# Kernel optimization log

Measured on AMD Instinct MI355X. Metric: run time of the kernel, lower is better.

Reference implementation:

```python
import jax, jax.numpy as jnp
import numpy as np

N, H = 8192, 128  # nodes, hidden_dim


def setup_inputs() -> dict:
    key = jax.random.key(0)
    ks = jax.random.split(key, 5)
    X = jax.random.normal(ks[0], (N, H), dtype=jnp.float32)
    adj = jax.random.uniform(ks[1], (N, N), dtype=jnp.float32)
    W1 = jax.random.normal(ks[2], (H, H), dtype=jnp.float32) / np.sqrt(H).astype(np.float32)
    b1 = jnp.zeros((H,), jnp.float32)
    W2 = jax.random.normal(ks[3], (H, H), dtype=jnp.float32) / np.sqrt(H).astype(np.float32)
    b2 = jnp.zeros((H,), jnp.float32)
    a = jax.random.normal(ks[4], (2 * H, 1), dtype=jnp.float32) * 0.1
    return {"X": X, "adj": adj, "W1": W1, "b1": b1, "W2": W2, "b2": b2, "a": a}


def reference(X, adj, W1, b1, W2, b2, a):
    n = X.shape[0]
    leaky = jax.nn.leaky_relu  # negative_slope = 0.01, matches torch defaults

    # --- GCN diffusion: A_hat = A + I, symmetric normalization, 3 hops ---
    A_hat = adj + jnp.eye(n, dtype=adj.dtype)
    dinv_sqrt = jax.lax.rsqrt(A_hat.sum(axis=1))
    A_norm = dinv_sqrt[:, None] * A_hat * dinv_sqrt[None, :]
    hA = A_norm @ X
    hA2 = A_norm @ hA
    hA3 = A_norm @ hA2
    hA, hA2, hA3 = leaky(hA), leaky(hA2), leaky(hA3)

    # --- scattering diffusion: lazy walk P = 0.5*(I + A D^-1), wavelets ---
    deg = adj.sum(axis=1)
    AD = adj / deg[None, :]  # A @ D^{-1} (column-normalized)

    def P(v):
        return 0.5 * (v + AD @ v)

    px = P(X)
    p2x = P(px)
    p3x = P(p2x)
    p4x = P(p3x)
    # moment = 1 -> |.|**1
    s1 = jnp.abs(X - px)      # Psi_1 = I - P
    s2 = jnp.abs(px - p2x)    # Psi_2 = P - P^2
    s3 = jnp.abs(p2x - p4x)   # Psi_3 = P^2 - P^4

    # --- 6-way attention fusion ---
    h_all = jnp.stack([hA, hA2, hA3, s1, s2, s3], axis=1)         # [N,6,H]
    h_rep = jnp.broadcast_to(X[:, None, :], h_all.shape)          # [N,6,H]
    a_input = jnp.concatenate([h_rep, h_all], axis=-1)            # [N,6,2H]
    e = jnp.einsum('nsk,ko->ns', jax.nn.relu(a_input), a)         # [N,6]
    attn = jax.nn.softmax(e, axis=1)                              # [N,6]
    h_prime = jnp.mean(attn[:, :, None] * h_all, axis=1)          # [N,H]

    # --- output MLP (Withgres=False, so gres layer is skipped) ---
    out = leaky(h_prime @ W1.T + b1)
    out = leaky(out @ W2.T + b2)
    return out
```

## Files before the change

kernel.cpp:

```cpp
#include <hip/hip_runtime.h>

typedef unsigned short ushort_t;
typedef unsigned int   uint_t;
typedef int   i32x4 __attribute__((ext_vector_type(4)));

typedef __attribute__((address_space(3))) void lds_void_t;
typedef __attribute__((address_space(1))) void gbl_void_t;

#define NN 8192
#define HH 128
#define KS 8
#define KLEN 1024
#define NTQ 16

__device__ __forceinline__ ushort_t f2bf(float x) {
    uint_t u = __float_as_uint(x);
    u += 0x7fffu + ((u >> 16) & 1u);
    return (ushort_t)(u >> 16);
}
__device__ __forceinline__ float bf2f(uint_t lo16) { return __uint_as_float(lo16 << 16); }
__device__ __forceinline__ float leaky(float x) { return x > 0.f ? x : 0.01f * x; }

__global__ __launch_bounds__(256) void conv_rowsum(const float* __restrict__ adj,
    char* __restrict__ adjq, float* __restrict__ s, float* __restrict__ rinv,
    float* __restrict__ zbase)
{
    const int i = blockIdx.x;
    if (i == 0) {
        ((float4*)zbase)[threadIdx.x] = float4{0.f, 0.f, 0.f, 0.f};
    }
    const float4* arow = (const float4*)(adj + ((size_t)i << 13));
    uint_t* brow = (uint_t*)(adjq + ((size_t)i << 13));
    float partial = 0.f;
    for (int t = threadIdx.x; t < 2048; t += 256) {
        const float4 v = arow[t];
        partial += (v.x + v.y) + (v.z + v.w);
        const uint_t q0 = (uint_t)__float2int_rn(v.x * 127.f);
        const uint_t q1 = (uint_t)__float2int_rn(v.y * 127.f);
        const uint_t q2 = (uint_t)__float2int_rn(v.z * 127.f);
        const uint_t q3 = (uint_t)__float2int_rn(v.w * 127.f);
        brow[t] = q0 | (q1 << 8) | (q2 << 16) | (q3 << 24);
    }
    #pragma unroll
    for (int off = 32; off; off >>= 1) partial += __shfl_xor(partial, off);
    __shared__ float ps[4];
    if ((threadIdx.x & 63) == 0) ps[threadIdx.x >> 6] = partial;
    __syncthreads();
    if (threadIdx.x == 0) {
        const float tot = (ps[0] + ps[1]) + (ps[2] + ps[3]);
        s[i]    = rsqrtf(tot + 1.0f);
        rinv[i] = 1.0f / tot;
    }
}

__global__ __launch_bounds__(256) void preMax(const float* __restrict__ u,
    const float* __restrict__ v, const float* __restrict__ s, const float* __restrict__ rinv,
    float* __restrict__ cmax)
{
    const int j0 = (blockIdx.x & 127) << 6;
    const int c0 = (blockIdx.x >> 7) << 6;
    __shared__ uint_t cm[64];
    if (threadIdx.x < 64) cm[threadIdx.x] = 0;
    __syncthreads();
    const int tx = threadIdx.x & 63;
    const int ty = threadIdx.x >> 6;
    float m = 0.f;
    #pragma unroll
    for (int rr = 0; rr < 16; ++rr) {
        const int j = j0 + ty + (rr << 2);
        const int c = c0 + tx;
        const float val = (c < 128) ? s[j] * u[((size_t)j << 7) + c]
                                    : rinv[j] * v[((size_t)j << 7) + (c - 128)];
        m = fmaxf(m, fabsf(val));
    }
    atomicMax(&cm[tx], __float_as_uint(m));
    __syncthreads();
    if (threadIdx.x < 64)
        atomicMax((uint_t*)&cmax[c0 + threadIdx.x], cm[threadIdx.x]);
}

__global__ __launch_bounds__(256) void preQ(const float* __restrict__ u,
    const float* __restrict__ v, const float* __restrict__ s, const float* __restrict__ rinv,
    const float* __restrict__ cmax, char* __restrict__ Bi8, float* __restrict__ dq)
{
    const int j0 = (blockIdx.x & 127) << 6;
    const int c0 = (blockIdx.x >> 7) << 6;
    __shared__ float tile[64][65];
    const int tx = threadIdx.x & 63;
    const int ty = threadIdx.x >> 6;
    #pragma unroll
    for (int rr = 0; rr < 16; ++rr) {
        const int jl = ty + (rr << 2);
        const int j = j0 + jl;
        const int c = c0 + tx;
        tile[jl][tx] = (c < 128) ? s[j] * u[((size_t)j << 7) + c]
                                 : rinv[j] * v[((size_t)j << 7) + (c - 128)];
    }
    __syncthreads();
    const int cl = threadIdx.x & 63;
    const int jq = threadIdx.x >> 6;
    const float cmv = cmax[c0 + cl];
    const float rs = cmv > 0.f ? 127.f / cmv : 0.f;
    uint_t w4[4];
    #pragma unroll
    for (int g = 0; g < 4; ++g) {
        uint_t wv = 0;
        #pragma unroll
        for (int b = 0; b < 4; ++b) {
            int q = __float2int_rn(tile[(jq << 4) + (g << 2) + b][cl] * rs);
            q = q > 127 ? 127 : (q < -127 ? -127 : q);
            wv |= ((uint_t)(q & 0xff)) << (8 * b);
        }
        w4[g] = wv;
    }
    uint4 st; st.x = w4[0]; st.y = w4[1]; st.z = w4[2]; st.w = w4[3];
    *(uint4*)(Bi8 + ((size_t)(c0 + cl) << 13) + j0 + (jq << 4)) = st;
    if ((blockIdx.x & 127) == 0 && threadIdx.x < 64)
        dq[c0 + threadIdx.x] = cmax[c0 + threadIdx.x] * (1.f / 16129.f);
}

#define WAITB(S) do {                                         \
    asm volatile("s_waitcnt " S ::: "memory");                \
    __builtin_amdgcn_sched_barrier(0);                        \
    __builtin_amdgcn_s_barrier();                             \
    __builtin_amdgcn_sched_barrier(0);                        \
} while (0)

__global__ __launch_bounds__(512, 2) void gemm_i8(const char* __restrict__ A,
    const char* __restrict__ Bt, ushort_t* __restrict__ Yb)
{
    __shared__ char lds[4 * 32768];
    const int bid = blockIdx.x;
    const int mb = bid & 31;
    const int ks = bid >> 5;
    const size_t mBase = (size_t)mb * 256;
    const int tid = threadIdx.x;
    const int w = tid >> 6, l = tid & 63;
    const int wr = w >> 2, wc = w & 3;
    const int frow = l & 15, fk = l >> 4;
    const int fsl = ((fk ^ ((frow >> 1) & 3)) << 4);
    const int srow = l >> 2;
    const int skoff = (((l & 3) ^ ((l >> 3) & 3)) << 4);
    const int kBeg = ks << 10;

    i32x4 acc[8][4] = {};

    auto STAGE = [&](int t) {
        const int k0 = kBeg + (t << 6);
        char* base = &lds[(t & 3) << 15];
        #pragma unroll
        for (int q = 0; q < 2; ++q) {
            const int c = (w << 1) + q;
            const int row = (c << 4) + srow;
            __builtin_amdgcn_global_load_lds(
                (const gbl_void_t*)(A + ((mBase + row) << 13) + k0 + skoff),
                (lds_void_t*)(base + (c << 10)), 16, 0, 0);
            __builtin_amdgcn_global_load_lds(
                (const gbl_void_t*)(Bt + ((size_t)row << 13) + k0 + skoff),
                (lds_void_t*)(base + 16384 + (c << 10)), 16, 0, 0);
        }
    };
    auto COMPUTE = [&](int T) {
        const char* buf = &lds[(T & 3) << 15];
        i32x4 av[8], bv[4];
        #pragma unroll
        for (int mi = 0; mi < 8; ++mi) {
            const int row = (wr << 7) + (mi << 4) + frow;
            av[mi] = *(const i32x4*)(buf + (row << 6) + fsl);
        }
        #pragma unroll
        for (int ni = 0; ni < 4; ++ni) {
            const int col = (wc << 6) + (ni << 4) + frow;
            bv[ni] = *(const i32x4*)(buf + 16384 + (col << 6) + fsl);
        }
        __builtin_amdgcn_s_setprio(1);
        #pragma unroll
        for (int mi = 0; mi < 8; ++mi)
            #pragma unroll
            for (int ni = 0; ni < 4; ++ni)
                acc[mi][ni] = __builtin_amdgcn_mfma_i32_16x16x64_i8(
                    av[mi], bv[ni], acc[mi][ni], 0, 0, 0);
        __builtin_amdgcn_s_setprio(0);
    };

    STAGE(0); STAGE(1); STAGE(2);
    #pragma unroll 1
    for (int T = 0; T < NTQ - 3; ++T) {
        WAITB("vmcnt(8)");
        STAGE(T + 3);
        COMPUTE(T);
    }
    WAITB("vmcnt(8)"); COMPUTE(NTQ - 3);
    WAITB("vmcnt(4)"); COMPUTE(NTQ - 2);
    WAITB("vmcnt(0)"); COMPUTE(NTQ - 1);
    __syncthreads();

    ushort_t* Cs = (ushort_t*)lds;
    const int orow = (l >> 4) << 2;
    const int ocol = l & 15;
    #pragma unroll
    for (int mi = 0; mi < 8; ++mi) {
        #pragma unroll
        for (int ni = 0; ni < 4; ++ni) {
            const int rl = (wr << 7) + (mi << 4) + orow;
            const int cl = (wc << 6) + (ni << 4) + ocol;
            #pragma unroll
            for (int r = 0; r < 4; ++r)
                Cs[(rl + r) * 256 + cl] = f2bf((float)acc[mi][ni][r]);
        }
    }
    __syncthreads();
    const size_t sliceBase = ((size_t)ks * NN + mBase) * 256;
    #pragma unroll
    for (int p = 0; p < 16; ++p) {
        const int idx16 = (p << 9) + tid;
        const int row   = idx16 >> 5;
        const int c16   = idx16 & 31;
        const uint4 v = *(const uint4*)(&Cs[(row << 8) + (c16 << 3)]);
        *(uint4*)(Yb + sliceBase + (size_t)row * 256 + (c16 << 3)) = v;
    }
}

__global__ __launch_bounds__(256, 2) void gemm_half_i8(const char* __restrict__ A,
    const char* __restrict__ Bt, ushort_t* __restrict__ Yb, int nbOff, int nbCount)
{
    __shared__ char lds[2 * 24576];
    const int bid  = blockIdx.x;
    const int mb   = bid & 31;
    const int rest = bid >> 5;
    const int nb   = nbOff + (rest % nbCount);
    const int ks   = rest / nbCount;
    const size_t mBase = (size_t)mb * 256;
    const size_t nBase = (size_t)nb * 128;
    const int tid = threadIdx.x;
    const int w = tid >> 6, l = tid & 63;
    const int wr = w >> 1, wc = w & 1;
    const int frow = l & 15, fk = l >> 4;
    const int fsl = ((fk ^ ((frow >> 1) & 3)) << 4);
    const int srow = l >> 2;
    const int skoff = (((l & 3) ^ ((l >> 3) & 3)) << 4);
    const int kBeg = ks << 10;

    i32x4 acc[8][4] = {};

    auto STAGE = [&](int t) {
        const int k0 = kBeg + (t << 6);
        char* base = &lds[(t & 1) * 24576];
        #pragma unroll
        for (int q = 0; q < 4; ++q) {
            const int c = (w << 2) + q;
            const int row = (c << 4) + srow;
            __builtin_amdgcn_global_load_lds(
                (const gbl_void_t*)(A + ((mBase + row) << 13) + k0 + skoff),
                (lds_void_t*)(base + (c << 10)), 16, 0, 0);
        }
        #pragma unroll
        for (int q = 0; q < 2; ++q) {
            const int c = (w << 1) + q;
            const int row = (c << 4) + srow;
            __builtin_amdgcn_global_load_lds(
                (const gbl_void_t*)(Bt + ((nBase + row) << 13) + k0 + skoff),
                (lds_void_t*)(base + 16384 + (c << 10)), 16, 0, 0);
        }
    };

    STAGE(0);
    __syncthreads();
    #pragma unroll 1
    for (int T = 0; T < NTQ; ++T) {
        if (T + 1 < NTQ) STAGE(T + 1);
        const char* buf = &lds[(T & 1) * 24576];
        i32x4 av[8], bv[4];
        #pragma unroll
        for (int mi = 0; mi < 8; ++mi) {
            const int row = (wr << 7) + (mi << 4) + frow;
            av[mi] = *(const i32x4*)(buf + (row << 6) + fsl);
        }
        #pragma unroll
        for (int ni = 0; ni < 4; ++ni) {
            const int col = (wc << 6) + (ni << 4) + frow;
            bv[ni] = *(const i32x4*)(buf + 16384 + (col << 6) + fsl);
        }
        __builtin_amdgcn_s_setprio(1);
        #pragma unroll
        for (int mi = 0; mi < 8; ++mi)
            #pragma unroll
            for (int ni = 0; ni < 4; ++ni)
                acc[mi][ni] = __builtin_amdgcn_mfma_i32_16x16x64_i8(
                    av[mi], bv[ni], acc[mi][ni], 0, 0, 0);
        __builtin_amdgcn_s_setprio(0);
        __syncthreads();
    }

    const int orow = (l >> 4) << 2;
    const int ocol = l & 15;
    const size_t sliceBase = ((size_t)ks * NN + mBase) * 256 + nBase;
    #pragma unroll
    for (int p = 0; p < 2; ++p) {
        __syncthreads();
        ushort_t* Cs = (ushort_t*)lds;
        #pragma unroll
        for (int mi = 0; mi < 4; ++mi) {
            #pragma unroll
            for (int ni = 0; ni < 4; ++ni) {
                const int rl = (wr << 6) + (mi << 4) + orow;
                const int cl = (wc << 6) + (ni << 4) + ocol;
                #pragma unroll
                for (int r = 0; r < 4; ++r)
                    Cs[(rl + r) * 128 + cl] = f2bf((float)acc[(p << 2) + mi][ni][r]);
            }
        }
        __syncthreads();
        #pragma unroll
        for (int pp = 0; pp < 8; ++pp) {
            const int idx16 = (pp << 8) + tid;
            const int lrow  = idx16 >> 4;
            const int c16   = idx16 & 15;
            const int rowIn = ((lrow >> 6) << 7) + (p << 6) + (lrow & 63);
            const uint4 v = *(const uint4*)(&Cs[(lrow << 7) + (c16 << 3)]);
            *(uint4*)(Yb + sliceBase + (size_t)rowIn * 256 + (c16 << 3)) = v;
        }
    }
}

__global__ __launch_bounds__(256) void reduce_post(const ushort_t* __restrict__ Yb,
    const float* __restrict__ u, const float* __restrict__ v,
    const float* __restrict__ s, const float* __restrict__ rinv,
    float* __restrict__ hop_out, float* __restrict__ walk_out,
    const float* __restrict__ dq, float* __restrict__ cmaxN, int c0Off)
{
    const int j0 = (blockIdx.x & 127) << 6;
    const int c0 = ((blockIdx.x >> 7) + c0Off) << 6;
    const bool hop = (c0 < 128);
    if (hop && hop_out == nullptr) return;
    __shared__ uint_t cm[64];
    if (cmaxN && threadIdx.x < 64) cm[threadIdx.x] = 0;
    if (cmaxN) __syncthreads();
    const int cg = threadIdx.x & 15;
    const int jr = threadIdx.x >> 4;
    const size_t SL = (size_t)NN * 256;
    const float4 dqv = ((const float4*)dq)[(c0 >> 2) + cg];
    float lm0 = 0.f, lm1 = 0.f, lm2 = 0.f, lm3 = 0.f;
    #pragma unroll
    for (int it = 0; it < 4; ++it) {
        const int jl = jr + (it << 4);
        const int j  = j0 + jl;
        const int c  = c0 + (cg << 2);
        const ushort_t* p = Yb + ((size_t)j << 8) + c;
        float e0 = 0.f, e1 = 0.f, e2 = 0.f, e3 = 0.f;
        #pragma unroll
        for (int kss = 0; kss < KS; ++kss) {
            const uint2 q = *(const uint2*)(p + kss * SL);
            e0 += bf2f(q.x & 0xffffu);
            e1 += __uint_as_float(q.x & 0xffff0000u);
            e2 += bf2f(q.y & 0xffffu);
            e3 += __uint_as_float(q.y & 0xffff0000u);
        }
        e0 *= dqv.x; e1 *= dqv.y; e2 *= dqv.z; e3 *= dqv.w;
        float4 o; float scale;
        if (hop) {
            const float si = s[j], si2 = si * si;
            const float4 uu = ((const float4*)u)[((size_t)j << 5) + (c >> 2)];
            o.x = si * e0 + si2 * uu.x;  o.y = si * e1 + si2 * uu.y;
            o.z = si * e2 + si2 * uu.z;  o.w = si * e3 + si2 * uu.w;
            ((float4*)hop_out)[((size_t)j << 5) + (c >> 2)] = o;
            scale = si;
        } else {
            const int cw = c - 128;
            const float4 vv = ((const float4*)v)[((size_t)j << 5) + (cw >> 2)];
            o.x = 0.5f * (vv.x + e0);  o.y = 0.5f * (vv.y + e1);
            o.z = 0.5f * (vv.z + e2);  o.w = 0.5f * (vv.w + e3);
            ((float4*)walk_out)[((size_t)j << 5) + (cw >> 2)] = o;
            scale = rinv[j];
        }
        if (cmaxN) {
            lm0 = fmaxf(lm0, fabsf(scale * o.x));
            lm1 = fmaxf(lm1, fabsf(scale * o.y));
            lm2 = fmaxf(lm2, fabsf(scale * o.z));
            lm3 = fmaxf(lm3, fabsf(scale * o.w));
        }
    }
    if (cmaxN) {
        atomicMax(&cm[(cg << 2) + 0], __float_as_uint(lm0));
        atomicMax(&cm[(cg << 2) + 1], __float_as_uint(lm1));
        atomicMax(&cm[(cg << 2) + 2], __float_as_uint(lm2));
        atomicMax(&cm[(cg << 2) + 3], __float_as_uint(lm3));
        __syncthreads();
        if (threadIdx.x < 64)
            atomicMax((uint_t*)&cmaxN[c0 + threadIdx.x], cm[threadIdx.x]);
    }
}

__global__ __launch_bounds__(256) void fuse_attn(const float* __restrict__ X,
    const float* __restrict__ hA, const float* __restrict__ hA2, const float* __restrict__ hA3,
    const float* __restrict__ px, const float* __restrict__ p2x, const float* __restrict__ p3x,
    const ushort_t* __restrict__ Yb, const float* __restrict__ dq,
    const float* __restrict__ a, float* __restrict__ hp)
{
    const int w = threadIdx.x >> 6, l = threadIdx.x & 63;
    const size_t i = (size_t)blockIdx.x * 4 + w;
    const size_t base = i << 7;
    const size_t SL = (size_t)NN * 256;
    float f[6][2];
    float e[6] = {0.f, 0.f, 0.f, 0.f, 0.f, 0.f};
    #pragma unroll
    for (int h = 0; h < 2; ++h) {
        const int k = l + (h << 6);
        const float a2 = a[128 + k];
        const float x   = X[base + k];
        const float t1  = leaky(hA [base + k]);
        const float t2  = leaky(hA2[base + k]);
        const float t3  = leaky(hA3[base + k]);
        const float pk  = px [base + k];
        const float p2k = p2x[base + k];
        const ushort_t* yp = Yb + (i << 8) + 128 + k;
        float ew = 0.f;
        #pragma unroll
        for (int kss = 0; kss < KS; ++kss) ew += bf2f(yp[kss * SL]);
        const float p4k = 0.5f * (p3x[base + k] + ew * dq[128 + k]);
        const float s1 = fabsf(x - pk);
        const float s2 = fabsf(pk - p2k);
        const float s3 = fabsf(p2k - p4k);
        f[0][h] = t1; f[1][h] = t2; f[2][h] = t3;
        f[3][h] = s1; f[4][h] = s2; f[5][h] = s3;
        e[0] += fmaxf(t1, 0.f) * a2;
        e[1] += fmaxf(t2, 0.f) * a2;
        e[2] += fmaxf(t3, 0.f) * a2;
        e[3] += s1 * a2;
        e[4] += s2 * a2;
        e[5] += s3 * a2;
    }
    #pragma unroll
    for (int ss = 0; ss < 6; ++ss) {
        #pragma unroll
        for (int off = 32; off; off >>= 1) e[ss] += __shfl_xor(e[ss], off);
    }
    float mx = e[0];
    #pragma unroll
    for (int ss = 1; ss < 6; ++ss) mx = fmaxf(mx, e[ss]);
    float at[6], sum = 0.f;
    #pragma unroll
    for (int ss = 0; ss < 6; ++ss) { at[ss] = expf(e[ss] - mx); sum += at[ss]; }
    const float inv = 1.f / (6.f * sum);
    #pragma unroll
    for (int h = 0; h < 2; ++h) {
        float o = 0.f;
        #pragma unroll
        for (int ss = 0; ss < 6; ++ss) o += at[ss] * f[ss][h];
        hp[base + l + (h << 6)] = o * inv;
    }
}

__global__ __launch_bounds__(256) void mlp(const float* __restrict__ Hm,
    const float* __restrict__ W, const float* __restrict__ b, float* __restrict__ out)
{
    __shared__ float Ws[128 * 140];
    __shared__ float Hs[16 * 140];
    const int node0 = blockIdx.x << 4;
    for (int rr = 0; rr < 64; ++rr) {
        const int idx = rr * 256 + threadIdx.x;
        Ws[(idx >> 7) * 140 + (idx & 127)] = W[idx];
    }
    #pragma unroll
    for (int rr = 0; rr < 8; ++rr) {
        const int idx = rr * 256 + threadIdx.x;
        Hs[(idx >> 7) * 140 + (idx & 127)] = Hm[((size_t)node0 << 7) + idx];
    }
    __syncthreads();
    const int c = threadIdx.x & 15;
    const int n = threadIdx.x >> 4;
    float acc[8] = {};
    for (int k4 = 0; k4 < 32; ++k4) {
        const float4 h4 = *(const float4*)(&Hs[n * 140 + (k4 << 2)]);
        #pragma unroll
        for (int r = 0; r < 8; ++r) {
            const float4 w4 = *(const float4*)(&Ws[(c + (r << 4)) * 140 + (k4 << 2)]);
            acc[r] += h4.x * w4.x + h4.y * w4.y + h4.z * w4.z + h4.w * w4.w;
        }
    }
    const size_t obase = ((size_t)(node0 + n)) << 7;
    #pragma unroll
    for (int r = 0; r < 8; ++r) {
        const int o = c + (r << 4);
        out[obase + o] = leaky(acc[r] + b[o]);
    }
}

extern "C" void kernel_launch(void* const* d_in, const int* in_sizes, int n_in,
                              void* d_out, int out_size, void* d_ws, size_t ws_size,
                              hipStream_t stream)
{
    const float* X   = (const float*)d_in[0];
    const float* adj = (const float*)d_in[1];
    const float* W1  = (const float*)d_in[2];
    const float* b1  = (const float*)d_in[3];
    const float* W2  = (const float*)d_in[4];
    const float* b2  = (const float*)d_in[5];
    const float* a   = (const float*)d_in[6];
    float* out = (float*)d_out;

    char* ws = (char*)d_ws;
    char*     adjq = ws;
    char*     Bi8  = ws + 67108864ull;
    ushort_t* Yb   = (ushort_t*)(ws + 69206016ull);
    float* hA  = (float*)(ws + 102760448ull);
    float* hA2 = hA  + 1048576;
    float* hA3 = hA2 + 1048576;
    float* px  = hA3 + 1048576;
    float* p2x = px  + 1048576;
    float* p3x = p2x + 1048576;
    float* p4x = p3x + 1048576;
    float* sbuf  = p4x + 1048576;
    float* rinvb = sbuf + 8192;
    float* cmaxb = rinvb + 8192;
    float* dq    = cmaxb + 1024;
    float* cmax1 = cmaxb, *cmax2 = cmaxb + 256, *cmax3 = cmaxb + 512, *cmax4 = cmaxb + 768;
    float* hp   = p4x;
    float* out1 = (float*)(ws + 69206016ull + 4194304ull);

    conv_rowsum<<<8192, 256, 0, stream>>>(adj, adjq, sbuf, rinvb, cmaxb);

    preMax<<<512, 256, 0, stream>>>(X, X, sbuf, rinvb, cmax1);
    preQ  <<<512, 256, 0, stream>>>(X, X, sbuf, rinvb, cmax1, Bi8, dq);
    gemm_i8<<<256, 512, 0, stream>>>(adjq, Bi8, Yb);
    reduce_post<<<512, 256, 0, stream>>>(Yb, X, X, sbuf, rinvb,
                                         hA, px, dq, cmax2, 0);
    preQ  <<<512, 256, 0, stream>>>(hA, px, sbuf, rinvb, cmax2, Bi8, dq);
    gemm_i8<<<256, 512, 0, stream>>>(adjq, Bi8, Yb);
    reduce_post<<<512, 256, 0, stream>>>(Yb, hA, px, sbuf, rinvb,
                                         hA2, p2x, dq, cmax3, 0);
    preQ  <<<512, 256, 0, stream>>>(hA2, p2x, sbuf, rinvb, cmax3, Bi8, dq);
    gemm_i8<<<256, 512, 0, stream>>>(adjq, Bi8, Yb);
    reduce_post<<<512, 256, 0, stream>>>(Yb, hA2, p2x, sbuf, rinvb,
                                         hA3, p3x, dq, cmax4, 0);
    preQ  <<<512, 256, 0, stream>>>(hA3, p3x, sbuf, rinvb, cmax4, Bi8, dq);
    gemm_half_i8<<<256, 256, 0, stream>>>(adjq, Bi8, Yb, 1, 1);

    fuse_attn<<<2048, 256, 0, stream>>>(X, hA, hA2, hA3, px, p2x, p3x,
                                        Yb, dq, a, hp);
    mlp<<<512, 256, 0, stream>>>(hp, W1, b1, out1);
    mlp<<<512, 256, 0, stream>>>(out1, W2, b2, out);
}
```

Baseline: 258.4 us.

## Fuse attention fusion and both MLP layers into one kernel

Merges the attention-weighting kernel and the two MLP launches into a single kernel that keeps per-node h_prime and the hidden activation in shared memory. This removes two launches and the global writes and reads of the intermediate hp and out1 buffers. Thread mapping changes to 16 threads per node with 8 features each, vectorising the bf16 partial-sum loads. The cost is fewer, heavier blocks and strided per-thread feature loads.

```diff
diff --git a/kernel.cpp b/kernel.cpp
--- a/kernel.cpp
+++ b/kernel.cpp
@@ -391,21 +391,41 @@
     }
 }
 
-__global__ __launch_bounds__(256) void fuse_attn(const float* __restrict__ X,
+__global__ __launch_bounds__(256) void attn_mlp(const float* __restrict__ X,
     const float* __restrict__ hA, const float* __restrict__ hA2, const float* __restrict__ hA3,
     const float* __restrict__ px, const float* __restrict__ p2x, const float* __restrict__ p3x,
     const ushort_t* __restrict__ Yb, const float* __restrict__ dq,
-    const float* __restrict__ a, float* __restrict__ hp)
-{
-    const int w = threadIdx.x >> 6, l = threadIdx.x & 63;
-    const size_t i = (size_t)blockIdx.x * 4 + w;
+    const float* __restrict__ a, const float* __restrict__ W1, const float* __restrict__ b1,
+    const float* __restrict__ W2, const float* __restrict__ b2, float* __restrict__ out)
+{
+    __shared__ float Ws[128 * 132];
+    __shared__ float Hs[16 * 132];
+    const int tid = threadIdx.x;
+    const int node0 = blockIdx.x << 4;
+    const int n = tid >> 4, c = tid & 15;
+    for (int rr = 0; rr < 64; ++rr) {
+        const int idx = rr * 256 + tid;
+        Ws[(idx >> 7) * 132 + (idx & 127)] = W1[idx];
+    }
+    const size_t i = (size_t)(node0 + n);
     const size_t base = i << 7;
+    const int k0 = c << 3;
     const size_t SL = (size_t)NN * 256;
-    float f[6][2];
+    float ew[8] = {};
+    const ushort_t* yp = Yb + (i << 8) + 128 + k0;
+    #pragma unroll
+    for (int kss = 0; kss < KS; ++kss) {
+        const uint4 q = *(const uint4*)(yp + kss * SL);
+        ew[0] += bf2f(q.x & 0xffffu);  ew[1] += __uint_as_float(q.x & 0xffff0000u);
+        ew[2] += bf2f(q.y & 0xffffu);  ew[3] += __uint_as_float(q.y & 0xffff0000u);
+        ew[4] += bf2f(q.z & 0xffffu);  ew[5] += __uint_as_float(q.z & 0xffff0000u);
+        ew[6] += bf2f(q.w & 0xffffu);  ew[7] += __uint_as_float(q.w & 0xffff0000u);
+    }
+    float f[6][8];
     float e[6] = {0.f, 0.f, 0.f, 0.f, 0.f, 0.f};
     #pragma unroll
-    for (int h = 0; h < 2; ++h) {
-        const int k = l + (h << 6);
+    for (int h = 0; h < 8; ++h) {
+        const int k = k0 + h;
         const float a2 = a[128 + k];
         const float x   = X[base + k];
         const float t1  = leaky(hA [base + k]);
@@ -413,11 +433,7 @@
         const float t3  = leaky(hA3[base + k]);
         const float pk  = px [base + k];
         const float p2k = p2x[base + k];
-        const ushort_t* yp = Yb + (i << 8) + 128 + k;
-        float ew = 0.f;
-        #pragma unroll
-        for (int kss = 0; kss < KS; ++kss) ew += bf2f(yp[kss * SL]);
-        const float p4k = 0.5f * (p3x[base + k] + ew * dq[128 + k]);
+        const float p4k = 0.5f * (p3x[base + k] + ew[h] * dq[128 + k]);
         const float s1 = fabsf(x - pk);
         const float s2 = fabsf(pk - p2k);
         const float s3 = fabsf(p2k - p4k);
@@ -433,7 +449,7 @@
     #pragma unroll
     for (int ss = 0; ss < 6; ++ss) {
         #pragma unroll
-        for (int off = 32; off; off >>= 1) e[ss] += __shfl_xor(e[ss], off);
+        for (int off = 8; off; off >>= 1) e[ss] += __shfl_xor(e[ss], off);
     }
     float mx = e[0];
     #pragma unroll
@@ -443,46 +459,46 @@
     for (int ss = 0; ss < 6; ++ss) { at[ss] = expf(e[ss] - mx); sum += at[ss]; }
     const float inv = 1.f / (6.f * sum);
     #pragma unroll
-    for (int h = 0; h < 2; ++h) {
+    for (int h = 0; h < 8; ++h) {
         float o = 0.f;
         #pragma unroll
         for (int ss = 0; ss < 6; ++ss) o += at[ss] * f[ss][h];
-        hp[base + l + (h << 6)] = o * inv;
-    }
-}
-
-__global__ __launch_bounds__(256) void mlp(const float* __restrict__ Hm,
-    const float* __restrict__ W, const float* __restrict__ b, float* __restrict__ out)
-{
-    __shared__ float Ws[128 * 140];
-    __shared__ float Hs[16 * 140];
-    const int node0 = blockIdx.x << 4;
-    for (int rr = 0; rr < 64; ++rr) {
-        const int idx = rr * 256 + threadIdx.x;
-        Ws[(idx >> 7) * 140 + (idx & 127)] = W[idx];
-    }
-    #pragma unroll
-    for (int rr = 0; rr < 8; ++rr) {
-        const int idx = rr * 256 + threadIdx.x;
-        Hs[(idx >> 7) * 140 + (idx & 127)] = Hm[((size_t)node0 << 7) + idx];
-    }
-    __syncthreads();
-    const int c = threadIdx.x & 15;
-    const int n = threadIdx.x >> 4;
+        Hs[n * 132 + k0 + h] = o * inv;
+    }
+    __syncthreads();
     float acc[8] = {};
     for (int k4 = 0; k4 < 32; ++k4) {
-        const float4 h4 = *(const float4*)(&Hs[n * 140 + (k4 << 2)]);
+        const float4 h4 = *(const float4*)(&Hs[n * 132 + (k4 << 2)]);
         #pragma unroll
         for (int r = 0; r < 8; ++r) {
-            const float4 w4 = *(const float4*)(&Ws[(c + (r << 4)) * 140 + (k4 << 2)]);
+            const float4 w4 = *(const float4*)(&Ws[(c + (r << 4)) * 132 + (k4 << 2)]);
             acc[r] += h4.x * w4.x + h4.y * w4.y + h4.z * w4.z + h4.w * w4.w;
         }
     }
-    const size_t obase = ((size_t)(node0 + n)) << 7;
+    __syncthreads();
     #pragma unroll
     for (int r = 0; r < 8; ++r) {
         const int o = c + (r << 4);
-        out[obase + o] = leaky(acc[r] + b[o]);
+        Hs[n * 132 + o] = leaky(acc[r] + b1[o]);
+    }
+    for (int rr = 0; rr < 64; ++rr) {
+        const int idx = rr * 256 + tid;
+        Ws[(idx >> 7) * 132 + (idx & 127)] = W2[idx];
+    }
+    __syncthreads();
+    float acc2[8] = {};
+    for (int k4 = 0; k4 < 32; ++k4) {
+        const float4 h4 = *(const float4*)(&Hs[n * 132 + (k4 << 2)]);
+        #pragma unroll
+        for (int r = 0; r < 8; ++r) {
+            const float4 w4 = *(const float4*)(&Ws[(c + (r << 4)) * 132 + (k4 << 2)]);
+            acc2[r] += h4.x * w4.x + h4.y * w4.y + h4.z * w4.z + h4.w * w4.w;
+        }
+    }
+    #pragma unroll
+    for (int r = 0; r < 8; ++r) {
+        const int o = c + (r << 4);
+        out[base + o] = leaky(acc2[r] + b2[o]);
     }
 }
 
@@ -509,14 +525,11 @@
     float* px  = hA3 + 1048576;
     float* p2x = px  + 1048576;
     float* p3x = p2x + 1048576;
-    float* p4x = p3x + 1048576;
-    float* sbuf  = p4x + 1048576;
+    float* sbuf  = p3x + 1048576;
     float* rinvb = sbuf + 8192;
     float* cmaxb = rinvb + 8192;
     float* dq    = cmaxb + 1024;
     float* cmax1 = cmaxb, *cmax2 = cmaxb + 256, *cmax3 = cmaxb + 512, *cmax4 = cmaxb + 768;
-    float* hp   = p4x;
-    float* out1 = (float*)(ws + 69206016ull + 4194304ull);
 
     conv_rowsum<<<8192, 256, 0, stream>>>(adj, adjq, sbuf, rinvb, cmaxb);
 
@@ -536,8 +549,6 @@
     preQ  <<<512, 256, 0, stream>>>(hA3, p3x, sbuf, rinvb, cmax4, Bi8, dq);
     gemm_half_i8<<<256, 256, 0, stream>>>(adjq, Bi8, Yb, 1, 1);
 
-    fuse_attn<<<2048, 256, 0, stream>>>(X, hA, hA2, hA3, px, p2x, p3x,
-                                        Yb, dq, a, hp);
-    mlp<<<512, 256, 0, stream>>>(hp, W1, b1, out1);
-    mlp<<<512, 256, 0, stream>>>(out1, W2, b2, out);
-}
+    attn_mlp<<<512, 256, 0, stream>>>(X, hA, hA2, hA3, px, p2x, p3x,
+                                      Yb, dq, a, W1, b1, W2, b2, out);
+}
```

Result: faster. 250.3 us (median of 2 runs) (-3.1%).
